# Kernel optimization log

Measured on AMD Instinct MI355X. Metric: run time of the kernel, lower is better.

Reference implementation:

```python
import jax, jax.numpy as jnp
import numpy as np

N_NODES = 100000
N_EDGES = 1200000
D_IN = 64
D_OUT = 64


def setup_inputs() -> dict:
    key = jax.random.key(0)
    k1, k2, k3, k4, k5 = jax.random.split(key, 5)
    x = jax.random.normal(k1, (N_NODES, D_IN), dtype=jnp.float32)
    # Xavier-uniform init for the [in, out] weight
    limit = float(np.sqrt(6.0 / (D_IN + D_OUT)))
    weight = jax.random.uniform(k2, (D_IN, D_OUT), dtype=jnp.float32,
                                minval=-limit, maxval=limit)
    edge_row = jnp.sort(jax.random.randint(k3, (N_EDGES,), 0, N_NODES, dtype=jnp.int32))
    edge_col = jax.random.randint(k4, (N_EDGES,), 0, N_NODES, dtype=jnp.int32)
    # positive values, as in a normalized adjacency
    edge_val = jax.random.uniform(k5, (N_EDGES,), dtype=jnp.float32)
    return {"x": x, "weight": weight, "edge_row": edge_row,
            "edge_col": edge_col, "edge_val": edge_val}


def reference(x, weight, edge_row, edge_col, edge_val):
    # dropout p=0.0 (eval) -> identity
    support = x @ weight                                  # [N, D_OUT]
    # spmm(adj, support): gather source rows, scale by edge value,
    # scatter-add into destination rows.
    msgs = support[edge_col] * edge_val[:, None]          # [E, D_OUT]
    output = jax.ops.segment_sum(msgs, edge_row, num_segments=N_NODES)
    return jax.nn.relu(output)
```

## Files before the change

### kernel.cpp

```cpp
#include <hip/hip_runtime.h>
#include <hip/hip_fp16.h>

#define D 64

__global__ __launch_bounds__(256, 3) void gemm_and_rowptr(
    const float* __restrict__ x, const float* __restrict__ w,
    __half* __restrict__ sup, int N,
    const int* __restrict__ erow, int* __restrict__ rptr, int E,
    int nGemmBlocks) {
  if ((int)blockIdx.x >= nGemmBlocks) {
    const int e = (blockIdx.x - nGemmBlocks) * 256 + threadIdx.x;
    if (e < E) {
      const int r = erow[e];
      const int rprev = (e == 0) ? -1 : erow[e - 1];
      for (int q = rprev + 1; q <= r; ++q) rptr[q] = e;
      if (e == E - 1)
        for (int q = r + 1; q <= N; ++q) rptr[q] = E;
    }
    return;
  }

  __shared__ alignas(16) float ws[D * D];
  __shared__ alignas(16) float xs[128 * D];
  const int tid = threadIdx.x;
  const int rowBase = blockIdx.x * 128;

#pragma unroll
  for (int i = 0; i < 4; ++i) {
    const int idx = i * 1024 + tid * 4;
    *(float4*)&ws[idx] = *(const float4*)&w[idx];
  }
#pragma unroll
  for (int i = 0; i < 8; ++i) {
    const int idx = i * 1024 + tid * 4;
    const int rl = idx >> 6;
    const int c = idx & 63;
    const int r = rowBase + rl;
    float4 v = make_float4(0.f, 0.f, 0.f, 0.f);
    if (r < N) v = *(const float4*)&x[(size_t)r * D + c];
    const int M = ((rl >> 2) & 15) << 2;
    *(float4*)&xs[rl * D + (c ^ M)] = v;
  }
  __syncthreads();

  const int cg = tid & 7;
  const int rg = tid >> 3;
  const int M = (rg & 15) << 2;
  const int cb = cg << 3;

  float4 A00 = make_float4(0.f, 0.f, 0.f, 0.f), A01 = A00;
  float4 A10 = A00, A11 = A00, A20 = A00, A21 = A00, A30 = A00, A31 = A00;

#pragma unroll 4
  for (int k = 0; k < D; ++k) {
    const float4 w0 = *(const float4*)&ws[k * D + cb];
    const float4 w1 = *(const float4*)&ws[k * D + cb + 4];
    const int kk = k ^ M;
    const float x0 = xs[(rg * 4 + 0) * D + kk];
    const float x1 = xs[(rg * 4 + 1) * D + kk];
    const float x2 = xs[(rg * 4 + 2) * D + kk];
    const float x3 = xs[(rg * 4 + 3) * D + kk];
    A00.x = fmaf(w0.x, x0, A00.x); A00.y = fmaf(w0.y, x0, A00.y);
    A00.z = fmaf(w0.z, x0, A00.z); A00.w = fmaf(w0.w, x0, A00.w);
    A01.x = fmaf(w1.x, x0, A01.x); A01.y = fmaf(w1.y, x0, A01.y);
    A01.z = fmaf(w1.z, x0, A01.z); A01.w = fmaf(w1.w, x0, A01.w);
    A10.x = fmaf(w0.x, x1, A10.x); A10.y = fmaf(w0.y, x1, A10.y);
    A10.z = fmaf(w0.z, x1, A10.z); A10.w = fmaf(w0.w, x1, A10.w);
    A11.x = fmaf(w1.x, x1, A11.x); A11.y = fmaf(w1.y, x1, A11.y);
    A11.z = fmaf(w1.z, x1, A11.z); A11.w = fmaf(w1.w, x1, A11.w);
    A20.x = fmaf(w0.x, x2, A20.x); A20.y = fmaf(w0.y, x2, A20.y);
    A20.z = fmaf(w0.z, x2, A20.z); A20.w = fmaf(w0.w, x2, A20.w);
    A21.x = fmaf(w1.x, x2, A21.x); A21.y = fmaf(w1.y, x2, A21.y);
    A21.z = fmaf(w1.z, x2, A21.z); A21.w = fmaf(w1.w, x2, A21.w);
    A30.x = fmaf(w0.x, x3, A30.x); A30.y = fmaf(w0.y, x3, A30.y);
    A30.z = fmaf(w0.z, x3, A30.z); A30.w = fmaf(w0.w, x3, A30.w);
    A31.x = fmaf(w1.x, x3, A31.x); A31.y = fmaf(w1.y, x3, A31.y);
    A31.z = fmaf(w1.z, x3, A31.z); A31.w = fmaf(w1.w, x3, A31.w);
  }

#define STORE_ROW(i, L, R)                                          \
  {                                                                 \
    const int r = rowBase + rg * 4 + (i);                           \
    if (r < N) {                                                    \
      __half2 h[4];                                                 \
      h[0] = __floats2half2_rn((L).x, (L).y);                       \
      h[1] = __floats2half2_rn((L).z, (L).w);                       \
      h[2] = __floats2half2_rn((R).x, (R).y);                       \
      h[3] = __floats2half2_rn((R).z, (R).w);                       \
      *(float4*)&sup[(size_t)r * D + cb] = *(float4*)h;             \
    }                                                               \
  }
  STORE_ROW(0, A00, A01)
  STORE_ROW(1, A10, A11)
  STORE_ROW(2, A20, A21)
  STORE_ROW(3, A30, A31)
#undef STORE_ROW
}

__global__ __launch_bounds__(256) void spmm_relu(
    const __half2* __restrict__ sup, const int* __restrict__ rp,
    const int* __restrict__ col, const float* __restrict__ val,
    float* __restrict__ out, int N) {
  const int lane = threadIdx.x & 63;
  const int g = lane >> 5;
  const int lp = lane & 31;
  const int r = blockIdx.x * 4 + (threadIdx.x >> 6);
  if (r >= N) return;
  const int s = __builtin_amdgcn_readfirstlane(rp[r]);
  const int e = __builtin_amdgcn_readfirstlane(rp[r + 1]);
  float ax = 0.f, ay = 0.f;
  int i = s;
  for (; i + 8 <= e; i += 8) {
#pragma unroll
    for (int u = 0; u < 4; ++u) {
      const int idx = i + 2 * u + g;
      const int c = col[idx];
      const float v = val[idx];
      const float2 f = __half22float2(sup[(size_t)c * 32 + lp]);
      ax = fmaf(f.x, v, ax);
      ay = fmaf(f.y, v, ay);
    }
  }
  for (; i + 2 <= e; i += 2) {
    const int idx = i + g;
    const int c = col[idx];
    const float v = val[idx];
    const float2 f = __half22float2(sup[(size_t)c * 32 + lp]);
    ax = fmaf(f.x, v, ax);
    ay = fmaf(f.y, v, ay);
  }
  if (i < e && g == 0) {
    const int c = col[i];
    const float v = val[i];
    const float2 f = __half22float2(sup[(size_t)c * 32 + lp]);
    ax = fmaf(f.x, v, ax);
    ay = fmaf(f.y, v, ay);
  }
  ax += __shfl_xor(ax, 32);
  ay += __shfl_xor(ay, 32);
  if (g == 0) {
    float2 o;
    o.x = fmaxf(ax, 0.f);
    o.y = fmaxf(ay, 0.f);
    *(float2*)&out[(size_t)r * D + lp * 2] = o;
  }
}

extern "C" void kernel_launch(void* const* d_in, const int* in_sizes, int n_in,
                              void* d_out, int out_size, void* d_ws, size_t ws_size,
                              hipStream_t stream) {
  const float* x = (const float*)d_in[0];
  const float* w = (const float*)d_in[1];
  const int* erow = (const int*)d_in[2];
  const int* ecol = (const int*)d_in[3];
  const float* eval = (const float*)d_in[4];
  float* out = (float*)d_out;

  const int N = in_sizes[0] / D;
  const int E = in_sizes[2];

  __half* sup = (__half*)d_ws;
  int* rp = (int*)((char*)d_ws + (((size_t)N * D * sizeof(__half) + 255) & ~(size_t)255));

  const int nGemmBlocks = (N + 127) / 128;
  const int nRpBlocks = (E + 255) / 256;

  gemm_and_rowptr<<<nGemmBlocks + nRpBlocks, 256, 0, stream>>>(
      x, w, sup, N, erow, rp, E, nGemmBlocks);
  spmm_relu<<<(N + 3) / 4, 256, 0, stream>>>((const __half2*)sup, rp, ecol, eval,
                                             out, N);
}
```

Measured before the change: 140.1 us.

## Process eight edges per wavefront with 16-byte gathers and shuffle-broadcast indices

The SpMM kernel now splits each 64-lane wavefront into eight groups of eight lanes. Each lane gathers a 16-byte chunk (eight halves) of a source row, so eight edges are processed in parallel instead of two. Column indices and values for the first 64 edges are loaded once with a coalesced read and broadcast through shuffles. The cost is a three-step cross-lane reduction and more accumulator registers per lane.

```diff
diff --git a/kernel.cpp b/kernel.cpp
--- a/kernel.cpp
+++ b/kernel.cpp
@@ -98,51 +98,84 @@
 }
 
 __global__ __launch_bounds__(256) void spmm_relu(
-    const __half2* __restrict__ sup, const int* __restrict__ rp,
-    const int* __restrict__ col, const float* __restrict__ val,
-    float* __restrict__ out, int N) {
+    const float4* __restrict__ sup4,
+    const int* __restrict__ rp, const int* __restrict__ col,
+    const float* __restrict__ val, float* __restrict__ out, int N) {
   const int lane = threadIdx.x & 63;
-  const int g = lane >> 5;
-  const int lp = lane & 31;
+  const int g = lane >> 3;
+  const int lg = lane & 7;
   const int r = blockIdx.x * 4 + (threadIdx.x >> 6);
   if (r >= N) return;
   const int s = __builtin_amdgcn_readfirstlane(rp[r]);
   const int e = __builtin_amdgcn_readfirstlane(rp[r + 1]);
-  float ax = 0.f, ay = 0.f;
-  int i = s;
-  for (; i + 8 <= e; i += 8) {
-#pragma unroll
-    for (int u = 0; u < 4; ++u) {
-      const int idx = i + 2 * u + g;
-      const int c = col[idx];
-      const float v = val[idx];
-      const float2 f = __half22float2(sup[(size_t)c * 32 + lp]);
-      ax = fmaf(f.x, v, ax);
-      ay = fmaf(f.y, v, ay);
+  const int deg = e - s;
+
+  int myc = 0;
+  float myv = 0.f;
+  if (lane < deg) {
+    myc = col[s + lane];
+    myv = val[s + lane];
+  }
+
+  float a0 = 0.f, a1 = 0.f, a2 = 0.f, a3 = 0.f;
+  float a4 = 0.f, a5 = 0.f, a6 = 0.f, a7 = 0.f;
+
+#define ACCUM(Q, V)                                                  \
+  {                                                                  \
+    const __half2* h = (const __half2*)&(Q);                         \
+    const float2 f0 = __half22float2(h[0]);                          \
+    const float2 f1 = __half22float2(h[1]);                          \
+    const float2 f2 = __half22float2(h[2]);                          \
+    const float2 f3 = __half22float2(h[3]);                          \
+    a0 = fmaf(f0.x, (V), a0); a1 = fmaf(f0.y, (V), a1);              \
+    a2 = fmaf(f1.x, (V), a2); a3 = fmaf(f1.y, (V), a3);              \
+    a4 = fmaf(f2.x, (V), a4); a5 = fmaf(f2.y, (V), a5);              \
+    a6 = fmaf(f3.x, (V), a6); a7 = fmaf(f3.y, (V), a7);              \
+  }
+
+  const int K = deg < 64 ? deg : 64;
+  for (int jb = 0; jb < K; jb += 16) {
+    const int j0 = jb + g;
+    const int j1 = jb + 8 + g;
+    int c0 = __shfl(myc, j0);
+    float v0 = __shfl(myv, j0);
+    int c1 = __shfl(myc, j1);
+    float v1 = __shfl(myv, j1);
+    if (j0 >= K) { c0 = 0; v0 = 0.f; }
+    if (j1 >= K) { c1 = 0; v1 = 0.f; }
+    const float4 q0 = sup4[(size_t)c0 * 8 + lg];
+    const float4 q1 = sup4[(size_t)c1 * 8 + lg];
+    ACCUM(q0, v0)
+    ACCUM(q1, v1)
+  }
+  for (int j = 64; j < deg; j += 8) {
+    int c = 0;
+    float v = 0.f;
+    if (j + g < deg) {
+      c = col[s + j + g];
+      v = val[s + j + g];
     }
-  }
-  for (; i + 2 <= e; i += 2) {
-    const int idx = i + g;
-    const int c = col[idx];
-    const float v = val[idx];
-    const float2 f = __half22float2(sup[(size_t)c * 32 + lp]);
-    ax = fmaf(f.x, v, ax);
-    ay = fmaf(f.y, v, ay);
-  }
-  if (i < e && g == 0) {
-    const int c = col[i];
-    const float v = val[i];
-    const float2 f = __half22float2(sup[(size_t)c * 32 + lp]);
-    ax = fmaf(f.x, v, ax);
-    ay = fmaf(f.y, v, ay);
-  }
-  ax += __shfl_xor(ax, 32);
-  ay += __shfl_xor(ay, 32);
+    const float4 q = sup4[(size_t)c * 8 + lg];
+    ACCUM(q, v)
+  }
+#undef ACCUM
+
+#define RED(x)            \
+  x += __shfl_xor(x, 8);  \
+  x += __shfl_xor(x, 16); \
+  x += __shfl_xor(x, 32);
+  RED(a0) RED(a1) RED(a2) RED(a3) RED(a4) RED(a5) RED(a6) RED(a7)
+#undef RED
+
   if (g == 0) {
-    float2 o;
-    o.x = fmaxf(ax, 0.f);
-    o.y = fmaxf(ay, 0.f);
-    *(float2*)&out[(size_t)r * D + lp * 2] = o;
+    float4 o0, o1;
+    o0.x = fmaxf(a0, 0.f); o0.y = fmaxf(a1, 0.f);
+    o0.z = fmaxf(a2, 0.f); o0.w = fmaxf(a3, 0.f);
+    o1.x = fmaxf(a4, 0.f); o1.y = fmaxf(a5, 0.f);
+    o1.z = fmaxf(a6, 0.f); o1.w = fmaxf(a7, 0.f);
+    float* po = &out[(size_t)r * D + lg * 8];
+    *(float4*)po = o0;
+    *(float4*)(po + 4) = o1;
   }
 }
 
@@ -167,6 +200,6 @@
 
   gemm_and_rowptr<<<nGemmBlocks + nRpBlocks, 256, 0, stream>>>(
       x, w, sup, N, erow, rp, E, nGemmBlocks);
-  spmm_relu<<<(N + 3) / 4, 256, 0, stream>>>((const __half2*)sup, rp, ecol, eval,
+  spmm_relu<<<(N + 3) / 4, 256, 0, stream>>>((const float4*)sup, rp, ecol, eval,
                                              out, N);
 }
```

Measured after the change: 133.1 us. 5.0% less time.

## Process two rows per wavefront with 8-lane edge groups and shuffled indices

Applied to the files above, without the earlier changes.

The SpMM kernel now gives each wavefront two destination rows and splits its 64 lanes into 8 groups of 8, so each lane gathers a 16-byte chunk of a half-precision support row. Column indices and values are loaded once per row with one coalesced read and broadcast by shuffles. A fast path covers both rows having degree at most 16 by issuing all four gathers up front. This aims to raise memory-level parallelism and cut index-load latency at average degree 12, at the cost of a longer three-step cross-lane reduction over eight accumulators.

```diff
diff --git a/kernel.cpp b/kernel.cpp
--- a/kernel.cpp
+++ b/kernel.cpp
@@ -97,54 +97,140 @@
 #undef STORE_ROW
 }
 
+
+#define DECL_ACC(p)                                                   \
+  float p##_0 = 0.f, p##_1 = 0.f, p##_2 = 0.f, p##_3 = 0.f,           \
+        p##_4 = 0.f, p##_5 = 0.f, p##_6 = 0.f, p##_7 = 0.f;
+
+#define ACCUM(p, Q, V)                                                \
+  {                                                                   \
+    const __half2* h_ = (const __half2*)&(Q);                         \
+    const float2 f0_ = __half22float2(h_[0]);                         \
+    const float2 f1_ = __half22float2(h_[1]);                         \
+    const float2 f2_ = __half22float2(h_[2]);                         \
+    const float2 f3_ = __half22float2(h_[3]);                         \
+    p##_0 = fmaf(f0_.x, (V), p##_0); p##_1 = fmaf(f0_.y, (V), p##_1); \
+    p##_2 = fmaf(f1_.x, (V), p##_2); p##_3 = fmaf(f1_.y, (V), p##_3); \
+    p##_4 = fmaf(f2_.x, (V), p##_4); p##_5 = fmaf(f2_.y, (V), p##_5); \
+    p##_6 = fmaf(f3_.x, (V), p##_6); p##_7 = fmaf(f3_.y, (V), p##_7); \
+  }
+
+#define REDUCE_STORE(p, r)                                            \
+  {                                                                   \
+    p##_0 += __shfl_xor(p##_0, 8);  p##_0 += __shfl_xor(p##_0, 16);   \
+    p##_0 += __shfl_xor(p##_0, 32);                                   \
+    p##_1 += __shfl_xor(p##_1, 8);  p##_1 += __shfl_xor(p##_1, 16);   \
+    p##_1 += __shfl_xor(p##_1, 32);                                   \
+    p##_2 += __shfl_xor(p##_2, 8);  p##_2 += __shfl_xor(p##_2, 16);   \
+    p##_2 += __shfl_xor(p##_2, 32);                                   \
+    p##_3 += __shfl_xor(p##_3, 8);  p##_3 += __shfl_xor(p##_3, 16);   \
+    p##_3 += __shfl_xor(p##_3, 32);                                   \
+    p##_4 += __shfl_xor(p##_4, 8);  p##_4 += __shfl_xor(p##_4, 16);   \
+    p##_4 += __shfl_xor(p##_4, 32);                                   \
+    p##_5 += __shfl_xor(p##_5, 8);  p##_5 += __shfl_xor(p##_5, 16);   \
+    p##_5 += __shfl_xor(p##_5, 32);                                   \
+    p##_6 += __shfl_xor(p##_6, 8);  p##_6 += __shfl_xor(p##_6, 16);   \
+    p##_6 += __shfl_xor(p##_6, 32);                                   \
+    p##_7 += __shfl_xor(p##_7, 8);  p##_7 += __shfl_xor(p##_7, 16);   \
+    p##_7 += __shfl_xor(p##_7, 32);                                   \
+    if (g == 0) {                                                     \
+      float4 o0, o1;                                                  \
+      o0.x = fmaxf(p##_0, 0.f); o0.y = fmaxf(p##_1, 0.f);             \
+      o0.z = fmaxf(p##_2, 0.f); o0.w = fmaxf(p##_3, 0.f);             \
+      o1.x = fmaxf(p##_4, 0.f); o1.y = fmaxf(p##_5, 0.f);             \
+      o1.z = fmaxf(p##_6, 0.f); o1.w = fmaxf(p##_7, 0.f);             \
+      float* po = &out[(size_t)(r)*D + lg * 8];                       \
+      *(float4*)po = o0;                                              \
+      *(float4*)(po + 4) = o1;                                        \
+    }                                                                 \
+  }
+
+#define ROW_GENERAL(r, s, deg, myc, myv)                              \
+  {                                                                   \
+    DECL_ACC(t)                                                       \
+    const int K = (deg) < 64 ? (deg) : 64;                            \
+    for (int jb = 0; jb < K; jb += 16) {                              \
+      const int j0 = jb + g, j1 = jb + 8 + g;                         \
+      int c0 = __shfl((myc), j0); float v0 = __shfl((myv), j0);       \
+      int c1 = __shfl((myc), j1); float v1 = __shfl((myv), j1);       \
+      if (j0 >= K) { c0 = 0; v0 = 0.f; }                              \
+      if (j1 >= K) { c1 = 0; v1 = 0.f; }                              \
+      const float4 q0 = sup4[(size_t)c0 * 8 + lg];                    \
+      const float4 q1 = sup4[(size_t)c1 * 8 + lg];                    \
+      ACCUM(t, q0, v0)                                                \
+      ACCUM(t, q1, v1)                                                \
+    }                                                                 \
+    for (int j = 64; j < (deg); j += 8) {                             \
+      int c = 0; float v = 0.f;                                       \
+      if (j + g < (deg)) { c = col[(s) + j + g]; v = val[(s) + j + g]; } \
+      const float4 q = sup4[(size_t)c * 8 + lg];                      \
+      ACCUM(t, q, v)                                                  \
+    }                                                                 \
+    REDUCE_STORE(t, r)                                                \
+  }
+
 __global__ __launch_bounds__(256) void spmm_relu(
-    const __half2* __restrict__ sup, const int* __restrict__ rp,
-    const int* __restrict__ col, const float* __restrict__ val,
-    float* __restrict__ out, int N) {
+    const float4* __restrict__ sup4,
+    const int* __restrict__ rp, const int* __restrict__ col,
+    const float* __restrict__ val, float* __restrict__ out, int N) {
   const int lane = threadIdx.x & 63;
-  const int g = lane >> 5;
-  const int lp = lane & 31;
-  const int r = blockIdx.x * 4 + (threadIdx.x >> 6);
-  if (r >= N) return;
-  const int s = __builtin_amdgcn_readfirstlane(rp[r]);
-  const int e = __builtin_amdgcn_readfirstlane(rp[r + 1]);
-  float ax = 0.f, ay = 0.f;
-  int i = s;
-  for (; i + 8 <= e; i += 8) {
-#pragma unroll
-    for (int u = 0; u < 4; ++u) {
-      const int idx = i + 2 * u + g;
-      const int c = col[idx];
-      const float v = val[idx];
-      const float2 f = __half22float2(sup[(size_t)c * 32 + lp]);
-      ax = fmaf(f.x, v, ax);
-      ay = fmaf(f.y, v, ay);
+  const int g = lane >> 3;
+  const int lg = lane & 7;
+  const int r0 = (blockIdx.x * 4 + (threadIdx.x >> 6)) * 2;
+  if (r0 >= N) return;
+  const int r1 = r0 + 1;
+  const bool has1 = r1 < N;
+
+  const int s0 = __builtin_amdgcn_readfirstlane(rp[r0]);
+  const int e0 = __builtin_amdgcn_readfirstlane(rp[r0 + 1]);
+  int e1 = e0;
+  if (has1) e1 = __builtin_amdgcn_readfirstlane(rp[r0 + 2]);
+  const int s1 = e0;
+  const int deg0 = e0 - s0;
+  const int deg1 = e1 - s1;
+
+  int myc0 = 0, myc1 = 0;
+  float myv0 = 0.f, myv1 = 0.f;
+  if (lane < deg0) { myc0 = col[s0 + lane]; myv0 = val[s0 + lane]; }
+  if (lane < deg1) { myc1 = col[s1 + lane]; myv1 = val[s1 + lane]; }
+
+  if (deg0 <= 16 && deg1 <= 16 && has1) {
+    const int j0 = g, j1 = 8 + g;
+    int c00 = __shfl(myc0, j0); float v00 = __shfl(myv0, j0);
+    int c01 = __shfl(myc0, j1); float v01 = __shfl(myv0, j1);
+    int c10 = __shfl(myc1, j0); float v10 = __shfl(myv1, j0);
+    int c11 = __shfl(myc1, j1); float v11 = __shfl(myv1, j1);
+    if (j0 >= deg0) { c00 = 0; v00 = 0.f; }
+    if (j1 >= deg0) { c01 = 0; v01 = 0.f; }
+    if (j0 >= deg1) { c10 = 0; v10 = 0.f; }
+    if (j1 >= deg1) { c11 = 0; v11 = 0.f; }
+    const float4 q00 = sup4[(size_t)c00 * 8 + lg];
+    const float4 q01 = sup4[(size_t)c01 * 8 + lg];
+    const float4 q10 = sup4[(size_t)c10 * 8 + lg];
+    const float4 q11 = sup4[(size_t)c11 * 8 + lg];
+    {
+      DECL_ACC(a)
+      ACCUM(a, q00, v00)
+      ACCUM(a, q01, v01)
+      REDUCE_STORE(a, r0)
     }
-  }
-  for (; i + 2 <= e; i += 2) {
-    const int idx = i + g;
-    const int c = col[idx];
-    const float v = val[idx];
-    const float2 f = __half22float2(sup[(size_t)c * 32 + lp]);
-    ax = fmaf(f.x, v, ax);
-    ay = fmaf(f.y, v, ay);
-  }
-  if (i < e && g == 0) {
-    const int c = col[i];
-    const float v = val[i];
-    const float2 f = __half22float2(sup[(size_t)c * 32 + lp]);
-    ax = fmaf(f.x, v, ax);
-    ay = fmaf(f.y, v, ay);
-  }
-  ax += __shfl_xor(ax, 32);
-  ay += __shfl_xor(ay, 32);
-  if (g == 0) {
-    float2 o;
-    o.x = fmaxf(ax, 0.f);
-    o.y = fmaxf(ay, 0.f);
-    *(float2*)&out[(size_t)r * D + lp * 2] = o;
-  }
+    {
+      DECL_ACC(b)
+      ACCUM(b, q10, v10)
+      ACCUM(b, q11, v11)
+      REDUCE_STORE(b, r1)
+    }
+    return;
+  }
+
+  ROW_GENERAL(r0, s0, deg0, myc0, myv0)
+  if (has1) ROW_GENERAL(r1, s1, deg1, myc1, myv1)
 }
+
+#undef ROW_GENERAL
+#undef REDUCE_STORE
+#undef ACCUM
+#undef DECL_ACC
 
 extern "C" void kernel_launch(void* const* d_in, const int* in_sizes, int n_in,
                               void* d_out, int out_size, void* d_ws, size_t ws_size,
@@ -167,6 +253,6 @@
 
   gemm_and_rowptr<<<nGemmBlocks + nRpBlocks, 256, 0, stream>>>(
       x, w, sup, N, erow, rp, E, nGemmBlocks);
-  spmm_relu<<<(N + 3) / 4, 256, 0, stream>>>((const __half2*)sup, rp, ecol, eval,
+  spmm_relu<<<(N + 7) / 8, 256, 0, stream>>>((const float4*)sup, rp, ecol, eval,
                                              out, N);
 }
```

Measured after the change: 132.9 us. 5.1% less time.

## Switch SpMM to edge-parallel blocks with shared-memory atomic accumulation

Applied to the files above, without the earlier changes.

Replaces the one-row-per-wavefront SpMM with blocks that own 64 destination rows and split their contiguous edge range across 32 groups of 8 threads. Each group gathers a full 128-byte fp16 support row as float4 loads and accumulates into a padded LDS tile with atomicAdd, then the block writes ReLU output with float4 stores. This targets load imbalance from variable row degrees and underused lanes in short rows, at the cost of LDS atomic traffic, an extra erow read per edge, and block-wide barriers.

```diff
diff --git a/kernel.cpp b/kernel.cpp
--- a/kernel.cpp
+++ b/kernel.cpp
@@ -97,52 +97,66 @@
 #undef STORE_ROW
 }
 
-__global__ __launch_bounds__(256) void spmm_relu(
-    const __half2* __restrict__ sup, const int* __restrict__ rp,
-    const int* __restrict__ col, const float* __restrict__ val,
+__global__ __launch_bounds__(256) void spmm_relu_v3(
+    const float4* __restrict__ sup4,
+    const int* __restrict__ rp, const int* __restrict__ erow,
+    const int* __restrict__ ecol, const float* __restrict__ eval,
     float* __restrict__ out, int N) {
-  const int lane = threadIdx.x & 63;
-  const int g = lane >> 5;
-  const int lp = lane & 31;
-  const int r = blockIdx.x * 4 + (threadIdx.x >> 6);
-  if (r >= N) return;
-  const int s = __builtin_amdgcn_readfirstlane(rp[r]);
-  const int e = __builtin_amdgcn_readfirstlane(rp[r + 1]);
-  float ax = 0.f, ay = 0.f;
-  int i = s;
-  for (; i + 8 <= e; i += 8) {
+  __shared__ float acc[64 * 65];
+  const int tid = threadIdx.x;
+
 #pragma unroll
-    for (int u = 0; u < 4; ++u) {
-      const int idx = i + 2 * u + g;
-      const int c = col[idx];
-      const float v = val[idx];
-      const float2 f = __half22float2(sup[(size_t)c * 32 + lp]);
-      ax = fmaf(f.x, v, ax);
-      ay = fmaf(f.y, v, ay);
+  for (int i = 0; i < 17; ++i) {
+    const int idx = i * 256 + tid;
+    if (idx < 64 * 65) acc[idx] = 0.f;
+  }
+  __syncthreads();
+
+  const int rowBase = blockIdx.x * 64;
+  const int rowEnd = (rowBase + 64 < N) ? rowBase + 64 : N;
+  const int s = __builtin_amdgcn_readfirstlane(rp[rowBase]);
+  const int e = __builtin_amdgcn_readfirstlane(rp[rowEnd]);
+
+  const int gid = tid >> 3;
+  const int lg = tid & 7;
+
+#pragma unroll 2
+  for (int i = s + gid; i < e; i += 32) {
+    const int r = erow[i] - rowBase;
+    const int c = ecol[i];
+    const float v = eval[i];
+    const float4 q = sup4[(size_t)c * 8 + lg];
+    const __half2* h = (const __half2*)&q;
+    const float2 f0 = __half22float2(h[0]);
+    const float2 f1 = __half22float2(h[1]);
+    const float2 f2 = __half22float2(h[2]);
+    const float2 f3 = __half22float2(h[3]);
+    float* a = &acc[r * 65 + lg * 8];
+    atomicAdd(&a[0], f0.x * v);
+    atomicAdd(&a[1], f0.y * v);
+    atomicAdd(&a[2], f1.x * v);
+    atomicAdd(&a[3], f1.y * v);
+    atomicAdd(&a[4], f2.x * v);
+    atomicAdd(&a[5], f2.y * v);
+    atomicAdd(&a[6], f3.x * v);
+    atomicAdd(&a[7], f3.y * v);
+  }
+  __syncthreads();
+
+#pragma unroll
+  for (int u = 0; u < 4; ++u) {
+    const int rl = u * 16 + (tid >> 4);
+    const int c4 = (tid & 15) * 4;
+    const int r = rowBase + rl;
+    if (r < N) {
+      const float* a = &acc[rl * 65 + c4];
+      float4 o;
+      o.x = fmaxf(a[0], 0.f);
+      o.y = fmaxf(a[1], 0.f);
+      o.z = fmaxf(a[2], 0.f);
+      o.w = fmaxf(a[3], 0.f);
+      *(float4*)&out[(size_t)r * D + c4] = o;
     }
-  }
-  for (; i + 2 <= e; i += 2) {
-    const int idx = i + g;
-    const int c = col[idx];
-    const float v = val[idx];
-    const float2 f = __half22float2(sup[(size_t)c * 32 + lp]);
-    ax = fmaf(f.x, v, ax);
-    ay = fmaf(f.y, v, ay);
-  }
-  if (i < e && g == 0) {
-    const int c = col[i];
-    const float v = val[i];
-    const float2 f = __half22float2(sup[(size_t)c * 32 + lp]);
-    ax = fmaf(f.x, v, ax);
-    ay = fmaf(f.y, v, ay);
-  }
-  ax += __shfl_xor(ax, 32);
-  ay += __shfl_xor(ay, 32);
-  if (g == 0) {
-    float2 o;
-    o.x = fmaxf(ax, 0.f);
-    o.y = fmaxf(ay, 0.f);
-    *(float2*)&out[(size_t)r * D + lp * 2] = o;
   }
 }
 
@@ -167,6 +181,6 @@
 
   gemm_and_rowptr<<<nGemmBlocks + nRpBlocks, 256, 0, stream>>>(
       x, w, sup, N, erow, rp, E, nGemmBlocks);
-  spmm_relu<<<(N + 3) / 4, 256, 0, stream>>>((const __half2*)sup, rp, ecol, eval,
-                                             out, N);
+  spmm_relu_v3<<<(N + 63) / 64, 256, 0, stream>>>(
+      (const float4*)sup, rp, erow, ecol, eval, out, N);
 }
```

Result: slower. 545.1 us (+289.0%).
